# Performance work log

Hardware: AMD Instinct MI355X
Metric: run time of the kernel (lower is better)

## Reference

```python
import jax, jax.numpy as jnp
from jax import lax
import numpy as np

KH, KW = 9, 9  # box-filter window (kernel=(9,9))
IN_CH = 1


def _box_sum(x):
    # F.conv2d(x, ones([1, in_ch, KH, KW]), stride=1, padding=(4, 4))
    k = jnp.ones((1, IN_CH, KH, KW), x.dtype)
    pad = ((KH - 1) // 2, (KH - 1) // 2), ((KW - 1) // 2, (KW - 1) // 2)
    return lax.conv_general_dilated(
        x, k, window_strides=(1, 1), padding=pad,
        dimension_numbers=("NCHW", "OIHW", "NCHW"))


def setup_inputs() -> dict:
    key = jax.random.key(0)
    k1, k2 = jax.random.split(key)
    B, C, H, W = 32, IN_CH, 512, 512
    inp = jax.random.normal(k1, (B, C, H, W), dtype=jnp.float32)
    tgt = jax.random.uniform(k2, (B, C, H, W), dtype=jnp.float32)
    return {"input": inp, "target": tgt}


def reference(input, target):
    # normalize target from [-1, 1] -> [0, 1]
    t = (target + 1.0) * 0.5
    II = input * input
    TT = t * t
    IT = input * t

    T_sum = _box_sum(t)
    I_sum = _box_sum(input)
    TT_sum = _box_sum(TT)
    II_sum = _box_sum(II)
    IT_sum = _box_sum(IT)

    ksize = float(KH * KW)
    Ihat = I_sum / ksize
    That = T_sum / ksize

    cross = IT_sum - Ihat * T_sum - That * I_sum + That * Ihat * ksize
    T_var = TT_sum - 2.0 * That * T_sum + That * That * ksize
    I_var = II_sum - 2.0 * Ihat * I_sum + Ihat * Ihat * ksize

    cc = cross * cross / (T_var * I_var + 1e-5)
    return -1.0 * jnp.mean(cc)
```

## Files before the change

### kernel.cpp

```cpp
#include <hip/hip_runtime.h>

#define IMG_H 512
#define IMG_W 512
#define N_IMG 32
#define ROWS  8
#define BANDS (IMG_H / ROWS)
#define NPIX  (32.0f * 512.0f * 512.0f)

__device__ __forceinline__ float dpp_left(float x) {
    return __int_as_float(__builtin_amdgcn_update_dpp(
        0, __float_as_int(x), 0x138, 0xf, 0xf, true));
}
__device__ __forceinline__ float dpp_right(float x) {
    return __int_as_float(__builtin_amdgcn_update_dpp(
        0, __float_as_int(x), 0x130, 0xf, 0xf, true));
}

template<bool EDGE>
__device__ __forceinline__ void load8t(const float* __restrict__ ip,
                                       const float* __restrict__ tp,
                                       int r, int c0, float* I, float* T) {
    const int rc = EDGE ? min(max(r, 0), IMG_H - 1) : r;
    const float* irow = ip + (ptrdiff_t)rc * IMG_W + c0;
    const float* trow = tp + (ptrdiff_t)rc * IMG_W + c0;
    float4 a = *(const float4*)(irow);
    float4 b = *(const float4*)(irow + 4);
    float4 c = *(const float4*)(trow);
    float4 d = *(const float4*)(trow + 4);
    I[0]=a.x; I[1]=a.y; I[2]=a.z; I[3]=a.w;
    I[4]=b.x; I[5]=b.y; I[6]=b.z; I[7]=b.w;
    T[0]=c.x; T[1]=c.y; T[2]=c.z; T[3]=c.w;
    T[4]=d.x; T[5]=d.y; T[6]=d.z; T[7]=d.w;
    if (EDGE) {
        const bool v = (r >= 0) && (r < IMG_H);
        #pragma unroll
        for (int j = 0; j < 8; ++j) {
            I[j] = v ? I[j] : 0.0f;
            T[j] = v ? T[j] : -1.0f;
        }
    }
}

__device__ __forceinline__ void slide_lead(const float* LI, const float* LTr,
                                           float* vI, float* vT, float* vII,
                                           float* vTT, float* vIT) {
    #pragma unroll
    for (int j = 0; j < 8; ++j) {
        float li = LI[j];
        float lt = fmaf(LTr[j], 0.5f, 0.5f);
        vI[j]  += li;
        vT[j]  += lt;
        vII[j]  = fmaf(li, li, vII[j]);
        vTT[j]  = fmaf(lt, lt, vTT[j]);
        vIT[j]  = fmaf(li, lt, vIT[j]);
    }
}

__device__ __forceinline__ void slide_full(const float* LI, const float* LTr,
                                           const float* QI, const float* QTr,
                                           float* vI, float* vT, float* vII,
                                           float* vTT, float* vIT) {
    #pragma unroll
    for (int j = 0; j < 8; ++j) {
        float li = LI[j], qi = QI[j];
        float lt = fmaf(LTr[j], 0.5f, 0.5f);
        float qt = fmaf(QTr[j], 0.5f, 0.5f);
        float dI = li - qi, aI = li + qi;
        float dT = lt - qt, aT = lt + qt;
        vI[j]  += dI;
        vT[j]  += dT;
        vII[j]  = fmaf(dI, aI, vII[j]);
        vTT[j]  = fmaf(dT, aT, vTT[j]);
        vIT[j]  = fmaf(li, lt, vIT[j] - qi * qt);
    }
}

__device__ __forceinline__ float cc_of(float sI, float sT, float sII, float sTT, float sIT) {
    const float inv81 = 1.0f / 81.0f;
    float u     = sI * inv81;
    float w     = sT * inv81;
    float cross = fmaf(-u, sT, sIT);
    float iv    = fmaf(-u, sI, sII);
    float tv    = fmaf(-w, sT, sTT);
    float den   = fmaf(tv, iv, 1e-5f);
    return cross * cross * __builtin_amdgcn_rcpf(den);
}

__device__ __forceinline__ float hphase(const float* vI, const float* vT,
                                        const float* vII, const float* vTT,
                                        const float* vIT) {
    float L0[4],R0[4],L1[4],R1[4],L2[4],R2[4],L3[4],R3[4],L4[4],R4[4];
    #pragma unroll
    for (int k = 0; k < 4; ++k) {
        L0[k] = dpp_left (vI [4+k]);  R0[k] = dpp_right(vI [k]);
        L1[k] = dpp_left (vT [4+k]);  R1[k] = dpp_right(vT [k]);
        L2[k] = dpp_left (vII[4+k]);  R2[k] = dpp_right(vII[k]);
        L3[k] = dpp_left (vTT[4+k]);  R3[k] = dpp_right(vTT[k]);
        L4[k] = dpp_left (vIT[4+k]);  R4[k] = dpp_right(vIT[k]);
    }
    float s0 = ((L0[0]+L0[1])+(L0[2]+L0[3])) + ((vI [0]+vI [1])+(vI [2]+vI [3])) + vI [4];
    float s1 = ((L1[0]+L1[1])+(L1[2]+L1[3])) + ((vT [0]+vT [1])+(vT [2]+vT [3])) + vT [4];
    float s2 = ((L2[0]+L2[1])+(L2[2]+L2[3])) + ((vII[0]+vII[1])+(vII[2]+vII[3])) + vII[4];
    float s3 = ((L3[0]+L3[1])+(L3[2]+L3[3])) + ((vTT[0]+vTT[1])+(vTT[2]+vTT[3])) + vTT[4];
    float s4 = ((L4[0]+L4[1])+(L4[2]+L4[3])) + ((vIT[0]+vIT[1])+(vIT[2]+vIT[3])) + vIT[4];
    float part = cc_of(s0, s1, s2, s3, s4);

    #define HSTEP(a0,a1,a2,a3,a4) \
        s0 += (a0); s1 += (a1); s2 += (a2); s3 += (a3); s4 += (a4); \
        part += cc_of(s0, s1, s2, s3, s4);

    HSTEP(vI[5]-L0[0], vT[5]-L1[0], vII[5]-L2[0], vTT[5]-L3[0], vIT[5]-L4[0])
    HSTEP(vI[6]-L0[1], vT[6]-L1[1], vII[6]-L2[1], vTT[6]-L3[1], vIT[6]-L4[1])
    HSTEP(vI[7]-L0[2], vT[7]-L1[2], vII[7]-L2[2], vTT[7]-L3[2], vIT[7]-L4[2])
    HSTEP(R0[0]-L0[3], R1[0]-L1[3], R2[0]-L2[3], R3[0]-L3[3], R4[0]-L4[3])
    HSTEP(R0[1]-vI[0], R1[1]-vT[0], R2[1]-vII[0], R3[1]-vTT[0], R4[1]-vIT[0])
    HSTEP(R0[2]-vI[1], R1[2]-vT[1], R2[2]-vII[1], R3[2]-vTT[1], R4[2]-vIT[1])
    HSTEP(R0[3]-vI[2], R1[3]-vT[2], R2[3]-vII[2], R3[3]-vTT[2], R4[3]-vIT[2])
    #undef HSTEP
    return part;
}

template<bool EDGE>
__device__ __forceinline__ float band_body(const float* __restrict__ ip,
                                           const float* __restrict__ tp,
                                           int r0, int c0) {
    float vI[8] = {}, vT[8] = {}, vII[8] = {}, vTT[8] = {}, vIT[8] = {};
    float acc = 0.0f;

    float ALI[8], ALT[8], AQI[8], AQT[8];
    float BLI[8], BLT[8], BQI[8], BQT[8];
    float CLI[8], CLT[8], DLI[8], DLT[8];

    load8t<EDGE>(ip, tp, r0 - 4, c0, ALI, ALT);
    load8t<EDGE>(ip, tp, r0 - 3, c0, BLI, BLT);
    load8t<EDGE>(ip, tp, r0 - 2, c0, CLI, CLT);
    load8t<EDGE>(ip, tp, r0 - 1, c0, DLI, DLT);

    slide_lead(ALI, ALT, vI, vT, vII, vTT, vIT);
    load8t<EDGE>(ip, tp, r0 + 0, c0, ALI, ALT);
    slide_lead(BLI, BLT, vI, vT, vII, vTT, vIT);
    load8t<EDGE>(ip, tp, r0 + 1, c0, BLI, BLT);
    slide_lead(CLI, CLT, vI, vT, vII, vTT, vIT);
    load8t<EDGE>(ip, tp, r0 + 2, c0, CLI, CLT);
    slide_lead(DLI, DLT, vI, vT, vII, vTT, vIT);
    load8t<EDGE>(ip, tp, r0 + 3, c0, DLI, DLT);

    slide_lead(ALI, ALT, vI, vT, vII, vTT, vIT);
    load8t<EDGE>(ip, tp, r0 + 4, c0, ALI, ALT);
    slide_lead(BLI, BLT, vI, vT, vII, vTT, vIT);
    load8t<EDGE>(ip, tp, r0 + 5, c0, BLI, BLT);
    load8t<EDGE>(ip, tp, r0 - 4, c0, BQI, BQT);
    slide_lead(CLI, CLT, vI, vT, vII, vTT, vIT);
    slide_lead(DLI, DLT, vI, vT, vII, vTT, vIT);

    slide_lead(ALI, ALT, vI, vT, vII, vTT, vIT);
    load8t<EDGE>(ip, tp, r0 + 6, c0, ALI, ALT);
    load8t<EDGE>(ip, tp, r0 - 3, c0, AQI, AQT);
    acc += hphase(vI, vT, vII, vTT, vIT);

    slide_full(BLI, BLT, BQI, BQT, vI, vT, vII, vTT, vIT);
    load8t<EDGE>(ip, tp, r0 + 7, c0, BLI, BLT);
    load8t<EDGE>(ip, tp, r0 - 2, c0, BQI, BQT);
    acc += hphase(vI, vT, vII, vTT, vIT);

    #pragma unroll 1
    for (int p = 1; p < 4; ++p) {
        const int k = 8 + 2 * p;
        slide_full(ALI, ALT, AQI, AQT, vI, vT, vII, vTT, vIT);
        load8t<EDGE>(ip, tp, r0 + k - 2,  c0, ALI, ALT);
        load8t<EDGE>(ip, tp, r0 + k - 11, c0, AQI, AQT);
        acc += hphase(vI, vT, vII, vTT, vIT);

        slide_full(BLI, BLT, BQI, BQT, vI, vT, vII, vTT, vIT);
        load8t<EDGE>(ip, tp, r0 + k - 1,  c0, BLI, BLT);
        load8t<EDGE>(ip, tp, r0 + k - 10, c0, BQI, BQT);
        acc += hphase(vI, vT, vII, vTT, vIT);
    }
    return acc;
}

__global__ __launch_bounds__(256)
void cc_loss_kernel(const float* __restrict__ in, const float* __restrict__ tg,
                    float* __restrict__ out) {
    __shared__ float red[4];

    const int t    = threadIdx.x;
    const int w    = t >> 6;
    const int lane = t & 63;

    const int bid  = blockIdx.x;
    const int bs   = (bid & 7) * 64 + (bid >> 3);

    const int gband = bs * 4 + w;
    const int b     = gband >> 6;
    const int band  = gband & 63;
    const int r0    = band * ROWS;
    const size_t base = (size_t)b * (IMG_H * IMG_W);
    const float* ip = in + base;
    const float* tp = tg + base;
    const int c0    = lane * 8;

    float acc;
    if (band >= 1 && band <= 62) acc = band_body<false>(ip, tp, r0, c0);
    else                         acc = band_body<true >(ip, tp, r0, c0);

    #pragma unroll
    for (int off = 32; off > 0; off >>= 1) acc += __shfl_down(acc, off, 64);
    if (lane == 0) red[w] = acc;
    __syncthreads();
    if (t == 0)
        atomicAdd(out, (red[0] + red[1] + red[2] + red[3]) * (-1.0f / NPIX));
}

extern "C" void kernel_launch(void* const* d_in, const int* in_sizes, int n_in,
                              void* d_out, int out_size, void* d_ws, size_t ws_size,
                              hipStream_t stream) {
    const float* in = (const float*)d_in[0];
    const float* tg = (const float*)d_in[1];
    float* out = (float*)d_out;

    hipMemsetAsync(out, 0, sizeof(float), stream);
    dim3 grid(N_IMG * BANDS / 4);
    cc_loss_kernel<<<grid, 256, 0, stream>>>(in, tg, out);
}
```

Measured before the change: 106.3 us.

## Halve band height to four rows, doubling grid and raising occupancy

```diff
diff --git a/kernel.cpp b/kernel.cpp
--- a/kernel.cpp
+++ b/kernel.cpp
@@ -3,15 +3,15 @@
 #define IMG_H 512
 #define IMG_W 512
 #define N_IMG 32
-#define ROWS  8
+#define ROWS  4
 #define BANDS (IMG_H / ROWS)
 #define NPIX  (32.0f * 512.0f * 512.0f)
 
-__device__ __forceinline__ float dpp_left(float x) {
+__device__ __forceinline__ float dl(float x) {
     return __int_as_float(__builtin_amdgcn_update_dpp(
         0, __float_as_int(x), 0x138, 0xf, 0xf, true));
 }
-__device__ __forceinline__ float dpp_right(float x) {
+__device__ __forceinline__ float dr(float x) {
     return __int_as_float(__builtin_amdgcn_update_dpp(
         0, __float_as_int(x), 0x130, 0xf, 0xf, true));
 }
@@ -89,33 +89,25 @@
 __device__ __forceinline__ float hphase(const float* vI, const float* vT,
                                         const float* vII, const float* vTT,
                                         const float* vIT) {
-    float L0[4],R0[4],L1[4],R1[4],L2[4],R2[4],L3[4],R3[4],L4[4],R4[4];
-    #pragma unroll
-    for (int k = 0; k < 4; ++k) {
-        L0[k] = dpp_left (vI [4+k]);  R0[k] = dpp_right(vI [k]);
-        L1[k] = dpp_left (vT [4+k]);  R1[k] = dpp_right(vT [k]);
-        L2[k] = dpp_left (vII[4+k]);  R2[k] = dpp_right(vII[k]);
-        L3[k] = dpp_left (vTT[4+k]);  R3[k] = dpp_right(vTT[k]);
-        L4[k] = dpp_left (vIT[4+k]);  R4[k] = dpp_right(vIT[k]);
-    }
-    float s0 = ((L0[0]+L0[1])+(L0[2]+L0[3])) + ((vI [0]+vI [1])+(vI [2]+vI [3])) + vI [4];
-    float s1 = ((L1[0]+L1[1])+(L1[2]+L1[3])) + ((vT [0]+vT [1])+(vT [2]+vT [3])) + vT [4];
-    float s2 = ((L2[0]+L2[1])+(L2[2]+L2[3])) + ((vII[0]+vII[1])+(vII[2]+vII[3])) + vII[4];
-    float s3 = ((L3[0]+L3[1])+(L3[2]+L3[3])) + ((vTT[0]+vTT[1])+(vTT[2]+vTT[3])) + vTT[4];
-    float s4 = ((L4[0]+L4[1])+(L4[2]+L4[3])) + ((vIT[0]+vIT[1])+(vIT[2]+vIT[3])) + vIT[4];
+    float s0 = ((dl(vI [4])+dl(vI [5]))+(dl(vI [6])+dl(vI [7]))) + ((vI [0]+vI [1])+(vI [2]+vI [3])) + vI [4];
+    float s1 = ((dl(vT [4])+dl(vT [5]))+(dl(vT [6])+dl(vT [7]))) + ((vT [0]+vT [1])+(vT [2]+vT [3])) + vT [4];
+    float s2 = ((dl(vII[4])+dl(vII[5]))+(dl(vII[6])+dl(vII[7]))) + ((vII[0]+vII[1])+(vII[2]+vII[3])) + vII[4];
+    float s3 = ((dl(vTT[4])+dl(vTT[5]))+(dl(vTT[6])+dl(vTT[7]))) + ((vTT[0]+vTT[1])+(vTT[2]+vTT[3])) + vTT[4];
+    float s4 = ((dl(vIT[4])+dl(vIT[5]))+(dl(vIT[6])+dl(vIT[7]))) + ((vIT[0]+vIT[1])+(vIT[2]+vIT[3])) + vIT[4];
     float part = cc_of(s0, s1, s2, s3, s4);
 
-    #define HSTEP(a0,a1,a2,a3,a4) \
-        s0 += (a0); s1 += (a1); s2 += (a2); s3 += (a3); s4 += (a4); \
+    #define HSTEP(e0,e1,e2,e3,e4) \
+        s0 += (e0); s1 += (e1); s2 += (e2); s3 += (e3); s4 += (e4); \
         part += cc_of(s0, s1, s2, s3, s4);
 
-    HSTEP(vI[5]-L0[0], vT[5]-L1[0], vII[5]-L2[0], vTT[5]-L3[0], vIT[5]-L4[0])
-    HSTEP(vI[6]-L0[1], vT[6]-L1[1], vII[6]-L2[1], vTT[6]-L3[1], vIT[6]-L4[1])
-    HSTEP(vI[7]-L0[2], vT[7]-L1[2], vII[7]-L2[2], vTT[7]-L3[2], vIT[7]-L4[2])
-    HSTEP(R0[0]-L0[3], R1[0]-L1[3], R2[0]-L2[3], R3[0]-L3[3], R4[0]-L4[3])
-    HSTEP(R0[1]-vI[0], R1[1]-vT[0], R2[1]-vII[0], R3[1]-vTT[0], R4[1]-vIT[0])
-    HSTEP(R0[2]-vI[1], R1[2]-vT[1], R2[2]-vII[1], R3[2]-vTT[1], R4[2]-vIT[1])
-    HSTEP(R0[3]-vI[2], R1[3]-vT[2], R2[3]-vII[2], R3[3]-vTT[2], R4[3]-vIT[2])
+    HSTEP(vI[5]-dl(vI[4]), vT[5]-dl(vT[4]), vII[5]-dl(vII[4]), vTT[5]-dl(vTT[4]), vIT[5]-dl(vIT[4]))
+    HSTEP(vI[6]-dl(vI[5]), vT[6]-dl(vT[5]), vII[6]-dl(vII[5]), vTT[6]-dl(vTT[5]), vIT[6]-dl(vIT[5]))
+    HSTEP(vI[7]-dl(vI[6]), vT[7]-dl(vT[6]), vII[7]-dl(vII[6]), vTT[7]-dl(vTT[6]), vIT[7]-dl(vIT[6]))
+    HSTEP(dr(vI[0])-dl(vI[7]), dr(vT[0])-dl(vT[7]), dr(vII[0])-dl(vII[7]),
+          dr(vTT[0])-dl(vTT[7]), dr(vIT[0])-dl(vIT[7]))
+    HSTEP(dr(vI[1])-vI[0], dr(vT[1])-vT[0], dr(vII[1])-vII[0], dr(vTT[1])-vTT[0], dr(vIT[1])-vIT[0])
+    HSTEP(dr(vI[2])-vI[1], dr(vT[2])-vT[1], dr(vII[2])-vII[1], dr(vTT[2])-vTT[1], dr(vIT[2])-vIT[1])
+    HSTEP(dr(vI[3])-vI[2], dr(vT[3])-vT[2], dr(vII[3])-vII[2], dr(vTT[3])-vTT[2], dr(vIT[3])-vIT[2])
     #undef HSTEP
     return part;
 }
@@ -129,57 +121,38 @@
 
     float ALI[8], ALT[8], AQI[8], AQT[8];
     float BLI[8], BLT[8], BQI[8], BQT[8];
-    float CLI[8], CLT[8], DLI[8], DLT[8];
 
     load8t<EDGE>(ip, tp, r0 - 4, c0, ALI, ALT);
     load8t<EDGE>(ip, tp, r0 - 3, c0, BLI, BLT);
-    load8t<EDGE>(ip, tp, r0 - 2, c0, CLI, CLT);
-    load8t<EDGE>(ip, tp, r0 - 1, c0, DLI, DLT);
-
-    slide_lead(ALI, ALT, vI, vT, vII, vTT, vIT);
-    load8t<EDGE>(ip, tp, r0 + 0, c0, ALI, ALT);
-    slide_lead(BLI, BLT, vI, vT, vII, vTT, vIT);
-    load8t<EDGE>(ip, tp, r0 + 1, c0, BLI, BLT);
-    slide_lead(CLI, CLT, vI, vT, vII, vTT, vIT);
-    load8t<EDGE>(ip, tp, r0 + 2, c0, CLI, CLT);
-    slide_lead(DLI, DLT, vI, vT, vII, vTT, vIT);
-    load8t<EDGE>(ip, tp, r0 + 3, c0, DLI, DLT);
-
-    slide_lead(ALI, ALT, vI, vT, vII, vTT, vIT);
-    load8t<EDGE>(ip, tp, r0 + 4, c0, ALI, ALT);
-    slide_lead(BLI, BLT, vI, vT, vII, vTT, vIT);
-    load8t<EDGE>(ip, tp, r0 + 5, c0, BLI, BLT);
-    load8t<EDGE>(ip, tp, r0 - 4, c0, BQI, BQT);
-    slide_lead(CLI, CLT, vI, vT, vII, vTT, vIT);
-    slide_lead(DLI, DLT, vI, vT, vII, vTT, vIT);
-
-    slide_lead(ALI, ALT, vI, vT, vII, vTT, vIT);
-    load8t<EDGE>(ip, tp, r0 + 6, c0, ALI, ALT);
-    load8t<EDGE>(ip, tp, r0 - 3, c0, AQI, AQT);
-    acc += hphase(vI, vT, vII, vTT, vIT);
-
-    slide_full(BLI, BLT, BQI, BQT, vI, vT, vII, vTT, vIT);
-    load8t<EDGE>(ip, tp, r0 + 7, c0, BLI, BLT);
-    load8t<EDGE>(ip, tp, r0 - 2, c0, BQI, BQT);
-    acc += hphase(vI, vT, vII, vTT, vIT);
 
     #pragma unroll 1
-    for (int p = 1; p < 4; ++p) {
-        const int k = 8 + 2 * p;
+    for (int p = 0; p < 4; ++p) {
+        slide_lead(ALI, ALT, vI, vT, vII, vTT, vIT);
+        load8t<EDGE>(ip, tp, r0 - 2 + 2*p, c0, ALI, ALT);
+        slide_lead(BLI, BLT, vI, vT, vII, vTT, vIT);
+        load8t<EDGE>(ip, tp, r0 - 1 + 2*p, c0, BLI, BLT);
+    }
+
+    #pragma unroll
+    for (int j = 0; j < 8; ++j) { AQI[j] = 0.0f; AQT[j] = -1.0f; }
+    load8t<EDGE>(ip, tp, r0 - 4, c0, BQI, BQT);
+
+    #pragma unroll 1
+    for (int p = 0; p < 2; ++p) {
         slide_full(ALI, ALT, AQI, AQT, vI, vT, vII, vTT, vIT);
-        load8t<EDGE>(ip, tp, r0 + k - 2,  c0, ALI, ALT);
-        load8t<EDGE>(ip, tp, r0 + k - 11, c0, AQI, AQT);
+        load8t<EDGE>(ip, tp, r0 + 6 + 2*p, c0, ALI, ALT);
+        load8t<EDGE>(ip, tp, r0 - 3 + 2*p, c0, AQI, AQT);
         acc += hphase(vI, vT, vII, vTT, vIT);
 
         slide_full(BLI, BLT, BQI, BQT, vI, vT, vII, vTT, vIT);
-        load8t<EDGE>(ip, tp, r0 + k - 1,  c0, BLI, BLT);
-        load8t<EDGE>(ip, tp, r0 + k - 10, c0, BQI, BQT);
+        load8t<EDGE>(ip, tp, r0 + 7 + 2*p, c0, BLI, BLT);
+        load8t<EDGE>(ip, tp, r0 - 2 + 2*p, c0, BQI, BQT);
         acc += hphase(vI, vT, vII, vTT, vIT);
     }
     return acc;
 }
 
-__global__ __launch_bounds__(256)
+__global__ __launch_bounds__(256, 4)
 void cc_loss_kernel(const float* __restrict__ in, const float* __restrict__ tg,
                     float* __restrict__ out) {
     __shared__ float red[4];
@@ -189,11 +162,11 @@
     const int lane = t & 63;
 
     const int bid  = blockIdx.x;
-    const int bs   = (bid & 7) * 64 + (bid >> 3);
+    const int bs   = (bid & 7) * 128 + (bid >> 3);
 
     const int gband = bs * 4 + w;
-    const int b     = gband >> 6;
-    const int band  = gband & 63;
+    const int b     = gband >> 7;
+    const int band  = gband & 127;
     const int r0    = band * ROWS;
     const size_t base = (size_t)b * (IMG_H * IMG_W);
     const float* ip = in + base;
@@ -201,8 +174,8 @@
     const int c0    = lane * 8;
 
     float acc;
-    if (band >= 1 && band <= 62) acc = band_body<false>(ip, tp, r0, c0);
-    else                         acc = band_body<true >(ip, tp, r0, c0);
+    if (band >= 1 && band <= 125) acc = band_body<false>(ip, tp, r0, c0);
+    else                          acc = band_body<true >(ip, tp, r0, c0);
 
     #pragma unroll
     for (int off = 32; off > 0; off >>= 1) acc += __shfl_down(acc, off, 64);
```

New measurement: 186.4 us. 1.75x slower.
